# Optimization experiments

Hardware: AMD Instinct MI355X
Metric: run time of the kernel (lower is better)

## Reference

```python
import jax, jax.numpy as jnp
import numpy as np

# Simulation constants (from module source)
RADIUS = 0.1
DT = 1.0 / 60.0
MAX_VEL = 0.5 * 0.1 / DT
NUM_ITERATIONS = 3
RELAXATION = 1.0
VISCOSITY = 60.0
DENSITY_REST = 17510.1
STIFFNESS = 2.99e-11
EPS = 1e-8
_SPIKY_C = 15.0 / (np.pi * RADIUS ** 6)  # spiky kernel normalization


def _cap_magnitude(A, cap):
    # torch: vv = cap/(||A||+1e-4); vv = min(vv, 1); A*vv
    vv = jnp.sqrt(jnp.sum(A * A, axis=-1, keepdims=True))
    s = jnp.minimum(cap / (vv + 1e-4), 1.0)
    return A * s


def setup_inputs() -> dict:
    key = jax.random.key(0)
    k1, k2 = jax.random.split(key)
    N = 4096
    locs = jax.random.uniform(k1, (1, N, 3), dtype=jnp.float32)  # unit box
    vel = 0.1 * jax.random.normal(k2, (1, N, 3), dtype=jnp.float32)
    return {"locs": locs, "vel": vel}


def _pairwise(pred):
    # pred: [B,N,3] -> diff [B,N,N,3], stable distance d [B,N,N], neighbor mask
    diff = pred[:, :, None, :] - pred[:, None, :, :]
    d2 = jnp.sum(diff * diff, axis=-1)
    d = jnp.sqrt(d2 + EPS)
    mask = (d < RADIUS) & (d2 > 1e-12)  # exclude self (include_self=False)
    return diff, d, mask


def reference(locs, vel):
    gravity = jnp.array([0.0, -9.8, 0.0], dtype=locs.dtype)
    # external forces + velocity clamp
    vel = vel + gravity * DT
    vel = _cap_magnitude(vel, MAX_VEL)
    pred = locs + DT * vel

    # position-based density constraint solver iterations
    for _ in range(NUM_ITERATIONS):
        diff, d, mask = _pairwise(pred)
        w = jnp.where(mask, _SPIKY_C * (RADIUS - d) ** 3, 0.0)       # spiky
        rho = jnp.sum(w, axis=-1)                                     # [B,N]
        lam = -(rho - DENSITY_REST) * STIFFNESS                       # [B,N]
        dw = jnp.where(mask, -3.0 * _SPIKY_C * (RADIUS - d) ** 2, 0.0)  # dspiky
        coef = (lam[:, :, None] + lam[:, None, :]) * dw / d           # [B,N,N]
        delta = jnp.einsum('bij,bijd->bid', coef, diff)
        pred = pred + delta / RELAXATION

    new_vel = (pred - locs) / DT

    # XSPH viscosity smoothing: dv_i = sum_j w_ij (v_j - v_i)
    _, d, mask = _pairwise(pred)
    w = jnp.where(mask, _SPIKY_C * (RADIUS - d) ** 3, 0.0)
    wsum = jnp.sum(w, axis=-1, keepdims=True)
    dv = jnp.einsum('bij,bjd->bid', w, new_vel) - wsum * new_vel
    new_vel = new_vel + VISCOSITY * DT * dv / DENSITY_REST
    new_vel = _cap_magnitude(new_vel, MAX_VEL)
    return pred, new_vel
```

## Files before the change

kernel.cpp:

```cpp
#include <hip/hip_runtime.h>
#include <math.h>

#define NMAX 4096
#define N4   (NMAX/4)


constexpr float RADIUS       = 0.1f;
constexpr float DT           = 1.0f / 60.0f;
constexpr float MAX_VEL      = 3.0f;
constexpr float VISCOSITY    = 60.0f;
constexpr float DENSITY_REST = 17510.1f;
constexpr float STIFFNESS    = 2.99e-11f;
constexpr float EPS          = 1e-8f;
constexpr float SPIKY_C      = (float)(15.0 / (3.14159265358979323846 * 1e-6));

__device__ __forceinline__ float elem(const float4& v, int c) {
    return reinterpret_cast<const float*>(&v)[c];
}

__global__ void k_predict(const float* __restrict__ locs, const float* __restrict__ vel,
                          float* __restrict__ px, float* __restrict__ py, float* __restrict__ pz,
                          int n) {
    int i = blockIdx.x * blockDim.x + threadIdx.x;
    if (i >= n) return;
    float vx = vel[3*i+0];
    float vy = vel[3*i+1] - 9.8f * DT;
    float vz = vel[3*i+2];
    float vv = sqrtf(vx*vx + vy*vy + vz*vz);
    float s  = fminf(MAX_VEL / (vv + 1e-4f), 1.0f);
    vx *= s; vy *= s; vz *= s;
    px[i] = locs[3*i+0] + DT * vx;
    py[i] = locs[3*i+1] + DT * vy;
    pz[i] = locs[3*i+2] + DT * vz;
}

__global__ __launch_bounds__(256) void k_rho(const float4* __restrict__ px, const float4* __restrict__ py,
                                             const float4* __restrict__ pz, float* __restrict__ Lam, int n) {
    __shared__ float4 sx[N4], sy[N4], sz[N4];
    int n4 = n >> 2;
    for (int idx = threadIdx.x; idx < n4; idx += 256) {
        sx[idx] = px[idx]; sy[idx] = py[idx]; sz[idx] = pz[idx];
    }
    __syncthreads();
    const int wave = threadIdx.x >> 6, lane = threadIdx.x & 63;
    const int i0 = blockIdx.x * 8 + wave * 2;
    if (i0 >= n) return;
    const float* fx = (const float*)sx; const float* fy = (const float*)sy; const float* fz = (const float*)sz;
    const float xi0 = fx[i0],   yi0 = fy[i0],   zi0 = fz[i0];
    const float xi1 = fx[i0+1], yi1 = fy[i0+1], zi1 = fz[i0+1];
    float S0 = 0.f, S1 = 0.f;
    for (int k = lane; k < n4; k += 64) {
        float4 X = sx[k], Y = sy[k], Z = sz[k];
#pragma unroll
        for (int c = 0; c < 4; ++c) {
            float xj = elem(X,c), yj = elem(Y,c), zj = elem(Z,c);
            {
                float dx = xi0-xj, dy = yi0-yj, dz = zi0-zj;
                float d2 = fmaf(dx,dx,EPS); d2 = fmaf(dy,dy,d2); d2 = fmaf(dz,dz,d2);
                float t  = fmaxf(RADIUS - __builtin_amdgcn_sqrtf(d2), 0.f);
                S0 = fmaf(t*t, t, S0);
            }
            {
                float dx = xi1-xj, dy = yi1-yj, dz = zi1-zj;
                float d2 = fmaf(dx,dx,EPS); d2 = fmaf(dy,dy,d2); d2 = fmaf(dz,dz,d2);
                float t  = fmaxf(RADIUS - __builtin_amdgcn_sqrtf(d2), 0.f);
                S1 = fmaf(t*t, t, S1);
            }
        }
    }
    for (int off = 32; off > 0; off >>= 1) {
        S0 += __shfl_down(S0, off);
        S1 += __shfl_down(S1, off);
    }
    if (lane == 0) {
        const float ts  = RADIUS - __builtin_amdgcn_sqrtf(EPS);
        const float TS3 = ts*ts*ts;
        const float k3  = 3.f * SPIKY_C * STIFFNESS;
        Lam[i0]   = k3 * (SPIKY_C * (S0 - TS3) - DENSITY_REST);
        Lam[i0+1] = k3 * (SPIKY_C * (S1 - TS3) - DENSITY_REST);
    }
}

__global__ __launch_bounds__(256) void k_delta(const float4* __restrict__ px, const float4* __restrict__ py,
                                               const float4* __restrict__ pz, const float4* __restrict__ Lm,
                                               float* __restrict__ qx, float* __restrict__ qy, float* __restrict__ qz,
                                               const float* __restrict__ locs,
                                               float* __restrict__ out_pred,
                                               float* __restrict__ vnx, float* __restrict__ vny, float* __restrict__ vnz,
                                               int n) {
    __shared__ float4 sx[N4], sy[N4], sz[N4], sl[N4];
    int n4 = n >> 2;
    for (int idx = threadIdx.x; idx < n4; idx += 256) {
        sx[idx] = px[idx]; sy[idx] = py[idx]; sz[idx] = pz[idx]; sl[idx] = Lm[idx];
    }
    __syncthreads();
    const int wave = threadIdx.x >> 6, lane = threadIdx.x & 63;
    const int i0 = blockIdx.x * 8 + wave * 2;
    if (i0 >= n) return;
    const float* fx = (const float*)sx; const float* fy = (const float*)sy;
    const float* fz = (const float*)sz; const float* fl = (const float*)sl;
    const float xi0 = fx[i0],   yi0 = fy[i0],   zi0 = fz[i0],   L0 = fl[i0];
    const float xi1 = fx[i0+1], yi1 = fy[i0+1], zi1 = fz[i0+1], L1 = fl[i0+1];
    float ax0=0.f, ay0=0.f, az0=0.f, ax1=0.f, ay1=0.f, az1=0.f;
    for (int k = lane; k < n4; k += 64) {
        float4 X = sx[k], Y = sy[k], Z = sz[k], L = sl[k];
#pragma unroll
        for (int c = 0; c < 4; ++c) {
            float xj = elem(X,c), yj = elem(Y,c), zj = elem(Z,c), Lj = elem(L,c);
            {
                float dx = xi0-xj, dy = yi0-yj, dz = zi0-zj;
                float d2 = fmaf(dx,dx,EPS); d2 = fmaf(dy,dy,d2); d2 = fmaf(dz,dz,d2);
                float rinv = __builtin_amdgcn_rsqf(d2);
                float t  = fmaxf(RADIUS - d2*rinv, 0.f);
                float cf = (L0 + Lj) * (t*t) * rinv;
                ax0 = fmaf(cf, dx, ax0); ay0 = fmaf(cf, dy, ay0); az0 = fmaf(cf, dz, az0);
            }
            {
                float dx = xi1-xj, dy = yi1-yj, dz = zi1-zj;
                float d2 = fmaf(dx,dx,EPS); d2 = fmaf(dy,dy,d2); d2 = fmaf(dz,dz,d2);
                float rinv = __builtin_amdgcn_rsqf(d2);
                float t  = fmaxf(RADIUS - d2*rinv, 0.f);
                float cf = (L1 + Lj) * (t*t) * rinv;
                ax1 = fmaf(cf, dx, ax1); ay1 = fmaf(cf, dy, ay1); az1 = fmaf(cf, dz, az1);
            }
        }
    }
    for (int off = 32; off > 0; off >>= 1) {
        ax0 += __shfl_down(ax0, off); ay0 += __shfl_down(ay0, off); az0 += __shfl_down(az0, off);
        ax1 += __shfl_down(ax1, off); ay1 += __shfl_down(ay1, off); az1 += __shfl_down(az1, off);
    }
    if (lane == 0) {
#pragma unroll
        for (int u = 0; u < 2; ++u) {
            int i = i0 + u;
            float nx_ = (u ? xi1+ax1 : xi0+ax0);
            float ny_ = (u ? yi1+ay1 : yi0+ay0);
            float nz_ = (u ? zi1+az1 : zi0+az0);
            qx[i] = nx_; qy[i] = ny_; qz[i] = nz_;
            if (out_pred) {
                out_pred[3*i+0] = nx_; out_pred[3*i+1] = ny_; out_pred[3*i+2] = nz_;
                vnx[i] = (nx_ - locs[3*i+0]) * (1.0f/DT);
                vny[i] = (ny_ - locs[3*i+1]) * (1.0f/DT);
                vnz[i] = (nz_ - locs[3*i+2]) * (1.0f/DT);
            }
        }
    }
}

__global__ __launch_bounds__(256) void k_visc(const float4* __restrict__ px, const float4* __restrict__ py,
                                              const float4* __restrict__ pz,
                                              const float4* __restrict__ vx, const float4* __restrict__ vy,
                                              const float4* __restrict__ vz,
                                              float* __restrict__ out, int n) {
    __shared__ float4 sx[N4/2], sy[N4/2], sz[N4/2], svx[N4/2], svy[N4/2], svz[N4/2];
    const int wave = threadIdx.x >> 6, lane = threadIdx.x & 63;
    const int i0 = blockIdx.x * 8 + wave * 2;
    const float* fpx = (const float*)px; const float* fpy = (const float*)py; const float* fpz = (const float*)pz;
    const float* fvx = (const float*)vx; const float* fvy = (const float*)vy; const float* fvz = (const float*)vz;
    const float xi0 = fpx[i0],   yi0 = fpy[i0],   zi0 = fpz[i0];
    const float xi1 = fpx[i0+1], yi1 = fpy[i0+1], zi1 = fpz[i0+1];
    const float vix0 = fvx[i0],   viy0 = fvy[i0],   viz0 = fvz[i0];
    const float vix1 = fvx[i0+1], viy1 = fvy[i0+1], viz1 = fvz[i0+1];
    float ws0=0.f, ax0=0.f, ay0=0.f, az0=0.f;
    float ws1=0.f, ax1=0.f, ay1=0.f, az1=0.f;
    const int n8 = n >> 3;
    for (int ch = 0; ch < 2; ++ch) {
        __syncthreads();
        for (int idx = threadIdx.x; idx < n8; idx += 256) {
            sx[idx]  = px[ch*n8+idx]; sy[idx]  = py[ch*n8+idx]; sz[idx]  = pz[ch*n8+idx];
            svx[idx] = vx[ch*n8+idx]; svy[idx] = vy[ch*n8+idx]; svz[idx] = vz[ch*n8+idx];
        }
        __syncthreads();
        for (int k = lane; k < n8; k += 64) {
            float4 X = sx[k], Y = sy[k], Z = sz[k], VX = svx[k], VY = svy[k], VZ = svz[k];
#pragma unroll
            for (int c = 0; c < 4; ++c) {
                float xj = elem(X,c), yj = elem(Y,c), zj = elem(Z,c);
                float vxj = elem(VX,c), vyj = elem(VY,c), vzj = elem(VZ,c);
                {
                    float dx = xi0-xj, dy = yi0-yj, dz = zi0-zj;
                    float d2 = fmaf(dx,dx,EPS); d2 = fmaf(dy,dy,d2); d2 = fmaf(dz,dz,d2);
                    float t  = fmaxf(RADIUS - __builtin_amdgcn_sqrtf(d2), 0.f);
                    float w  = t*t*t;
                    ws0 += w;
                    ax0 = fmaf(w, vxj, ax0); ay0 = fmaf(w, vyj, ay0); az0 = fmaf(w, vzj, az0);
                }
                {
                    float dx = xi1-xj, dy = yi1-yj, dz = zi1-zj;
                    float d2 = fmaf(dx,dx,EPS); d2 = fmaf(dy,dy,d2); d2 = fmaf(dz,dz,d2);
                    float t  = fmaxf(RADIUS - __builtin_amdgcn_sqrtf(d2), 0.f);
                    float w  = t*t*t;
                    ws1 += w;
                    ax1 = fmaf(w, vxj, ax1); ay1 = fmaf(w, vyj, ay1); az1 = fmaf(w, vzj, az1);
                }
            }
        }
    }
    for (int off = 32; off > 0; off >>= 1) {
        ws0 += __shfl_down(ws0, off); ax0 += __shfl_down(ax0, off);
        ay0 += __shfl_down(ay0, off); az0 += __shfl_down(az0, off);
        ws1 += __shfl_down(ws1, off); ax1 += __shfl_down(ax1, off);
        ay1 += __shfl_down(ay1, off); az1 += __shfl_down(az1, off);
    }
    if (lane == 0 && i0 < n) {
        constexpr float K = VISCOSITY * DT / DENSITY_REST;
        const float KC = K * SPIKY_C;
#pragma unroll
        for (int u = 0; u < 2; ++u) {
            int i = i0 + u;
            float vix = (u ? vix1 : vix0), viy = (u ? viy1 : viy0), viz = (u ? viz1 : viz0);
            float sw  = (u ? ws1 : ws0);
            float sax = (u ? ax1 : ax0), say = (u ? ay1 : ay0), saz = (u ? az1 : az0);
            float nvx = vix + KC * (sax - sw * vix);
            float nvy = viy + KC * (say - sw * viy);
            float nvz = viz + KC * (saz - sw * viz);
            float vv = sqrtf(nvx*nvx + nvy*nvy + nvz*nvz);
            float s  = fminf(MAX_VEL / (vv + 1e-4f), 1.0f);
            out[3*n + 3*i + 0] = nvx * s;
            out[3*n + 3*i + 1] = nvy * s;
            out[3*n + 3*i + 2] = nvz * s;
        }
    }
}

extern "C" void kernel_launch(void* const* d_in, const int* in_sizes, int n_in,
                              void* d_out, int out_size, void* d_ws, size_t ws_size,
                              hipStream_t stream) {
    const float* locs = (const float*)d_in[0];
    const float* vel  = (const float*)d_in[1];
    float* out = (float*)d_out;
    int n = in_sizes[0] / 3;

    float* w = (float*)d_ws;
    float* p0x = w;          float* p0y = p0x + n;  float* p0z = p0y + n;
    float* p1x = p0z + n;    float* p1y = p1x + n;  float* p1z = p1y + n;
    float* lam = p1z + n;
    float* vnx = lam + n;    float* vny = vnx + n;  float* vnz = vny + n;

    int nb = n / 8;

    k_predict<<<(n + 255) / 256, 256, 0, stream>>>(locs, vel, p0x, p0y, p0z, n);

    k_rho<<<nb, 256, 0, stream>>>((const float4*)p0x, (const float4*)p0y, (const float4*)p0z, lam, n);
    k_delta<<<nb, 256, 0, stream>>>((const float4*)p0x, (const float4*)p0y, (const float4*)p0z,
                                    (const float4*)lam, p1x, p1y, p1z,
                                    locs, nullptr, nullptr, nullptr, nullptr, n);
    k_rho<<<nb, 256, 0, stream>>>((const float4*)p1x, (const float4*)p1y, (const float4*)p1z, lam, n);
    k_delta<<<nb, 256, 0, stream>>>((const float4*)p1x, (const float4*)p1y, (const float4*)p1z,
                                    (const float4*)lam, p0x, p0y, p0z,
                                    locs, nullptr, nullptr, nullptr, nullptr, n);
    k_rho<<<nb, 256, 0, stream>>>((const float4*)p0x, (const float4*)p0y, (const float4*)p0z, lam, n);
    k_delta<<<nb, 256, 0, stream>>>((const float4*)p0x, (const float4*)p0y, (const float4*)p0z,
                                    (const float4*)lam, p1x, p1y, p1z,
                                    locs, out, vnx, vny, vnz, n);
    k_visc<<<nb, 256, 0, stream>>>((const float4*)p1x, (const float4*)p1y, (const float4*)p1z,
                                   (const float4*)vnx, (const float4*)vny, (const float4*)vnz, out, n);
}
```

Measured before the change: 123.9 us.

## Fuse predict, solver iterations and viscosity into one cooperative kernel

Merges the predict, the three density/delta iterations and the XSPH viscosity kernels into a single cooperative kernel that uses grid-wide syncs between phases. It also updates positions in place, replacing the double buffer. The aim is to remove eight kernel launches and the gaps between them. In exchange it adds seven grid barriers and a fixed 64KB shared-memory footprint per block, which may lower occupancy. It also relies on all n/8 blocks being co-resident for the cooperative launch.

```diff
diff --git a/kernel.cpp b/kernel.cpp
--- a/kernel.cpp
+++ b/kernel.cpp
@@ -1,5 +1,8 @@
 #include <hip/hip_runtime.h>
+#include <hip/hip_cooperative_groups.h>
 #include <math.h>
+
+namespace cg = cooperative_groups;
 
 #define NMAX 4096
 #define N4   (NMAX/4)
@@ -18,167 +21,163 @@
     return reinterpret_cast<const float*>(&v)[c];
 }
 
-__global__ void k_predict(const float* __restrict__ locs, const float* __restrict__ vel,
-                          float* __restrict__ px, float* __restrict__ py, float* __restrict__ pz,
-                          int n) {
-    int i = blockIdx.x * blockDim.x + threadIdx.x;
-    if (i >= n) return;
-    float vx = vel[3*i+0];
-    float vy = vel[3*i+1] - 9.8f * DT;
-    float vz = vel[3*i+2];
-    float vv = sqrtf(vx*vx + vy*vy + vz*vz);
-    float s  = fminf(MAX_VEL / (vv + 1e-4f), 1.0f);
-    vx *= s; vy *= s; vz *= s;
-    px[i] = locs[3*i+0] + DT * vx;
-    py[i] = locs[3*i+1] + DT * vy;
-    pz[i] = locs[3*i+2] + DT * vz;
-}
-
-__global__ __launch_bounds__(256) void k_rho(const float4* __restrict__ px, const float4* __restrict__ py,
-                                             const float4* __restrict__ pz, float* __restrict__ Lam, int n) {
-    __shared__ float4 sx[N4], sy[N4], sz[N4];
-    int n4 = n >> 2;
-    for (int idx = threadIdx.x; idx < n4; idx += 256) {
-        sx[idx] = px[idx]; sy[idx] = py[idx]; sz[idx] = pz[idx];
-    }
-    __syncthreads();
-    const int wave = threadIdx.x >> 6, lane = threadIdx.x & 63;
-    const int i0 = blockIdx.x * 8 + wave * 2;
-    if (i0 >= n) return;
-    const float* fx = (const float*)sx; const float* fy = (const float*)sy; const float* fz = (const float*)sz;
-    const float xi0 = fx[i0],   yi0 = fy[i0],   zi0 = fz[i0];
-    const float xi1 = fx[i0+1], yi1 = fy[i0+1], zi1 = fz[i0+1];
-    float S0 = 0.f, S1 = 0.f;
-    for (int k = lane; k < n4; k += 64) {
-        float4 X = sx[k], Y = sy[k], Z = sz[k];
-#pragma unroll
-        for (int c = 0; c < 4; ++c) {
-            float xj = elem(X,c), yj = elem(Y,c), zj = elem(Z,c);
-            {
-                float dx = xi0-xj, dy = yi0-yj, dz = zi0-zj;
-                float d2 = fmaf(dx,dx,EPS); d2 = fmaf(dy,dy,d2); d2 = fmaf(dz,dz,d2);
-                float t  = fmaxf(RADIUS - __builtin_amdgcn_sqrtf(d2), 0.f);
-                S0 = fmaf(t*t, t, S0);
-            }
-            {
-                float dx = xi1-xj, dy = yi1-yj, dz = zi1-zj;
-                float d2 = fmaf(dx,dx,EPS); d2 = fmaf(dy,dy,d2); d2 = fmaf(dz,dz,d2);
-                float t  = fmaxf(RADIUS - __builtin_amdgcn_sqrtf(d2), 0.f);
-                S1 = fmaf(t*t, t, S1);
-            }
-        }
-    }
-    for (int off = 32; off > 0; off >>= 1) {
-        S0 += __shfl_down(S0, off);
-        S1 += __shfl_down(S1, off);
-    }
-    if (lane == 0) {
-        const float ts  = RADIUS - __builtin_amdgcn_sqrtf(EPS);
-        const float TS3 = ts*ts*ts;
-        const float k3  = 3.f * SPIKY_C * STIFFNESS;
-        Lam[i0]   = k3 * (SPIKY_C * (S0 - TS3) - DENSITY_REST);
-        Lam[i0+1] = k3 * (SPIKY_C * (S1 - TS3) - DENSITY_REST);
-    }
-}
-
-__global__ __launch_bounds__(256) void k_delta(const float4* __restrict__ px, const float4* __restrict__ py,
-                                               const float4* __restrict__ pz, const float4* __restrict__ Lm,
-                                               float* __restrict__ qx, float* __restrict__ qy, float* __restrict__ qz,
-                                               const float* __restrict__ locs,
-                                               float* __restrict__ out_pred,
-                                               float* __restrict__ vnx, float* __restrict__ vny, float* __restrict__ vnz,
-                                               int n) {
-    __shared__ float4 sx[N4], sy[N4], sz[N4], sl[N4];
-    int n4 = n >> 2;
-    for (int idx = threadIdx.x; idx < n4; idx += 256) {
-        sx[idx] = px[idx]; sy[idx] = py[idx]; sz[idx] = pz[idx]; sl[idx] = Lm[idx];
-    }
-    __syncthreads();
-    const int wave = threadIdx.x >> 6, lane = threadIdx.x & 63;
-    const int i0 = blockIdx.x * 8 + wave * 2;
-    if (i0 >= n) return;
-    const float* fx = (const float*)sx; const float* fy = (const float*)sy;
-    const float* fz = (const float*)sz; const float* fl = (const float*)sl;
-    const float xi0 = fx[i0],   yi0 = fy[i0],   zi0 = fz[i0],   L0 = fl[i0];
-    const float xi1 = fx[i0+1], yi1 = fy[i0+1], zi1 = fz[i0+1], L1 = fl[i0+1];
-    float ax0=0.f, ay0=0.f, az0=0.f, ax1=0.f, ay1=0.f, az1=0.f;
-    for (int k = lane; k < n4; k += 64) {
-        float4 X = sx[k], Y = sy[k], Z = sz[k], L = sl[k];
-#pragma unroll
-        for (int c = 0; c < 4; ++c) {
-            float xj = elem(X,c), yj = elem(Y,c), zj = elem(Z,c), Lj = elem(L,c);
-            {
-                float dx = xi0-xj, dy = yi0-yj, dz = zi0-zj;
-                float d2 = fmaf(dx,dx,EPS); d2 = fmaf(dy,dy,d2); d2 = fmaf(dz,dz,d2);
-                float rinv = __builtin_amdgcn_rsqf(d2);
-                float t  = fmaxf(RADIUS - d2*rinv, 0.f);
-                float cf = (L0 + Lj) * (t*t) * rinv;
-                ax0 = fmaf(cf, dx, ax0); ay0 = fmaf(cf, dy, ay0); az0 = fmaf(cf, dz, az0);
-            }
-            {
-                float dx = xi1-xj, dy = yi1-yj, dz = zi1-zj;
-                float d2 = fmaf(dx,dx,EPS); d2 = fmaf(dy,dy,d2); d2 = fmaf(dz,dz,d2);
-                float rinv = __builtin_amdgcn_rsqf(d2);
-                float t  = fmaxf(RADIUS - d2*rinv, 0.f);
-                float cf = (L1 + Lj) * (t*t) * rinv;
-                ax1 = fmaf(cf, dx, ax1); ay1 = fmaf(cf, dy, ay1); az1 = fmaf(cf, dz, az1);
-            }
-        }
-    }
-    for (int off = 32; off > 0; off >>= 1) {
-        ax0 += __shfl_down(ax0, off); ay0 += __shfl_down(ay0, off); az0 += __shfl_down(az0, off);
-        ax1 += __shfl_down(ax1, off); ay1 += __shfl_down(ay1, off); az1 += __shfl_down(az1, off);
-    }
-    if (lane == 0) {
-#pragma unroll
-        for (int u = 0; u < 2; ++u) {
-            int i = i0 + u;
-            float nx_ = (u ? xi1+ax1 : xi0+ax0);
-            float ny_ = (u ? yi1+ay1 : yi0+ay0);
-            float nz_ = (u ? zi1+az1 : zi0+az0);
-            qx[i] = nx_; qy[i] = ny_; qz[i] = nz_;
-            if (out_pred) {
-                out_pred[3*i+0] = nx_; out_pred[3*i+1] = ny_; out_pred[3*i+2] = nz_;
-                vnx[i] = (nx_ - locs[3*i+0]) * (1.0f/DT);
-                vny[i] = (ny_ - locs[3*i+1]) * (1.0f/DT);
-                vnz[i] = (nz_ - locs[3*i+2]) * (1.0f/DT);
-            }
-        }
-    }
-}
-
-__global__ __launch_bounds__(256) void k_visc(const float4* __restrict__ px, const float4* __restrict__ py,
-                                              const float4* __restrict__ pz,
-                                              const float4* __restrict__ vx, const float4* __restrict__ vy,
-                                              const float4* __restrict__ vz,
-                                              float* __restrict__ out, int n) {
-    __shared__ float4 sx[N4/2], sy[N4/2], sz[N4/2], svx[N4/2], svy[N4/2], svz[N4/2];
-    const int wave = threadIdx.x >> 6, lane = threadIdx.x & 63;
-    const int i0 = blockIdx.x * 8 + wave * 2;
-    const float* fpx = (const float*)px; const float* fpy = (const float*)py; const float* fpz = (const float*)pz;
-    const float* fvx = (const float*)vx; const float* fvy = (const float*)vy; const float* fvz = (const float*)vz;
-    const float xi0 = fpx[i0],   yi0 = fpy[i0],   zi0 = fpz[i0];
-    const float xi1 = fpx[i0+1], yi1 = fpy[i0+1], zi1 = fpz[i0+1];
-    const float vix0 = fvx[i0],   viy0 = fvy[i0],   viz0 = fvz[i0];
-    const float vix1 = fvx[i0+1], viy1 = fvy[i0+1], viz1 = fvz[i0+1];
+__global__ __launch_bounds__(256) void k_fused(
+        const float* __restrict__ locs, const float* __restrict__ vel,
+        float* __restrict__ px, float* __restrict__ py, float* __restrict__ pz,
+        float* __restrict__ lam,
+        float* __restrict__ vnx, float* __restrict__ vny, float* __restrict__ vnz,
+        float* __restrict__ out, int n) {
+    cg::grid_group grid = cg::this_grid();
+    __shared__ float4 smem[4 * N4];
+    float4* sx = smem;
+    float4* sy = smem + N4;
+    float4* sz = smem + 2 * N4;
+    float4* sl = smem + 3 * N4;
+    const int tid  = threadIdx.x;
+    const int wave = tid >> 6, lane = tid & 63;
+    const int i0   = blockIdx.x * 8 + wave * 2;
+    const int n4   = n >> 2;
+
+    {
+        int i = blockIdx.x * 256 + tid;
+        if (i < n) {
+            float vx = vel[3*i+0];
+            float vy = vel[3*i+1] - 9.8f * DT;
+            float vz = vel[3*i+2];
+            float vv = sqrtf(vx*vx + vy*vy + vz*vz);
+            float s  = fminf(MAX_VEL / (vv + 1e-4f), 1.0f);
+            px[i] = locs[3*i+0] + DT * vx * s;
+            py[i] = locs[3*i+1] + DT * vy * s;
+            pz[i] = locs[3*i+2] + DT * vz * s;
+        }
+    }
+    grid.sync();
+
+    for (int it = 0; it < 3; ++it) {
+        for (int idx = tid; idx < n4; idx += 256) {
+            sx[idx] = ((const float4*)px)[idx];
+            sy[idx] = ((const float4*)py)[idx];
+            sz[idx] = ((const float4*)pz)[idx];
+        }
+        __syncthreads();
+
+        const float* fx = (const float*)sx; const float* fy = (const float*)sy;
+        const float* fz = (const float*)sz; const float* fl = (const float*)sl;
+        const float xi0 = fx[i0],   yi0 = fy[i0],   zi0 = fz[i0];
+        const float xi1 = fx[i0+1], yi1 = fy[i0+1], zi1 = fz[i0+1];
+
+        float S0 = 0.f, S1 = 0.f;
+        for (int k = lane; k < n4; k += 64) {
+            float4 X = sx[k], Y = sy[k], Z = sz[k];
+#pragma unroll
+            for (int c = 0; c < 4; ++c) {
+                float xj = elem(X,c), yj = elem(Y,c), zj = elem(Z,c);
+                {
+                    float dx = xi0-xj, dy = yi0-yj, dz = zi0-zj;
+                    float d2 = fmaf(dx,dx,EPS); d2 = fmaf(dy,dy,d2); d2 = fmaf(dz,dz,d2);
+                    float t  = fmaxf(RADIUS - __builtin_amdgcn_sqrtf(d2), 0.f);
+                    S0 = fmaf(t*t, t, S0);
+                }
+                {
+                    float dx = xi1-xj, dy = yi1-yj, dz = zi1-zj;
+                    float d2 = fmaf(dx,dx,EPS); d2 = fmaf(dy,dy,d2); d2 = fmaf(dz,dz,d2);
+                    float t  = fmaxf(RADIUS - __builtin_amdgcn_sqrtf(d2), 0.f);
+                    S1 = fmaf(t*t, t, S1);
+                }
+            }
+        }
+        for (int off = 32; off > 0; off >>= 1) {
+            S0 += __shfl_down(S0, off);
+            S1 += __shfl_down(S1, off);
+        }
+        if (lane == 0) {
+            const float ts  = RADIUS - __builtin_amdgcn_sqrtf(EPS);
+            const float TS3 = ts*ts*ts;
+            const float k3  = 3.f * SPIKY_C * STIFFNESS;
+            lam[i0]   = k3 * (SPIKY_C * (S0 - TS3) - DENSITY_REST);
+            lam[i0+1] = k3 * (SPIKY_C * (S1 - TS3) - DENSITY_REST);
+        }
+        grid.sync();
+
+        for (int idx = tid; idx < n4; idx += 256) sl[idx] = ((const float4*)lam)[idx];
+        __syncthreads();
+
+        const float L0 = fl[i0], L1 = fl[i0+1];
+        float ax0=0.f, ay0=0.f, az0=0.f, ax1=0.f, ay1=0.f, az1=0.f;
+        for (int k = lane; k < n4; k += 64) {
+            float4 X = sx[k], Y = sy[k], Z = sz[k], L = sl[k];
+#pragma unroll
+            for (int c = 0; c < 4; ++c) {
+                float xj = elem(X,c), yj = elem(Y,c), zj = elem(Z,c), Lj = elem(L,c);
+                {
+                    float dx = xi0-xj, dy = yi0-yj, dz = zi0-zj;
+                    float d2 = fmaf(dx,dx,EPS); d2 = fmaf(dy,dy,d2); d2 = fmaf(dz,dz,d2);
+                    float rinv = __builtin_amdgcn_rsqf(d2);
+                    float t  = fmaxf(RADIUS - d2*rinv, 0.f);
+                    float cf = (L0 + Lj) * (t*t) * rinv;
+                    ax0 = fmaf(cf, dx, ax0); ay0 = fmaf(cf, dy, ay0); az0 = fmaf(cf, dz, az0);
+                }
+                {
+                    float dx = xi1-xj, dy = yi1-yj, dz = zi1-zj;
+                    float d2 = fmaf(dx,dx,EPS); d2 = fmaf(dy,dy,d2); d2 = fmaf(dz,dz,d2);
+                    float rinv = __builtin_amdgcn_rsqf(d2);
+                    float t  = fmaxf(RADIUS - d2*rinv, 0.f);
+                    float cf = (L1 + Lj) * (t*t) * rinv;
+                    ax1 = fmaf(cf, dx, ax1); ay1 = fmaf(cf, dy, ay1); az1 = fmaf(cf, dz, az1);
+                }
+            }
+        }
+        for (int off = 32; off > 0; off >>= 1) {
+            ax0 += __shfl_down(ax0, off); ay0 += __shfl_down(ay0, off); az0 += __shfl_down(az0, off);
+            ax1 += __shfl_down(ax1, off); ay1 += __shfl_down(ay1, off); az1 += __shfl_down(az1, off);
+        }
+        if (lane == 0) {
+#pragma unroll
+            for (int u = 0; u < 2; ++u) {
+                int i = i0 + u;
+                float nx_ = (u ? xi1+ax1 : xi0+ax0);
+                float ny_ = (u ? yi1+ay1 : yi0+ay0);
+                float nz_ = (u ? zi1+az1 : zi0+az0);
+                px[i] = nx_; py[i] = ny_; pz[i] = nz_;
+                if (it == 2) {
+                    out[3*i+0] = nx_; out[3*i+1] = ny_; out[3*i+2] = nz_;
+                    vnx[i] = (nx_ - locs[3*i+0]) * (1.0f/DT);
+                    vny[i] = (ny_ - locs[3*i+1]) * (1.0f/DT);
+                    vnz[i] = (nz_ - locs[3*i+2]) * (1.0f/DT);
+                }
+            }
+        }
+        grid.sync();
+    }
+
+    const int n8 = n >> 3;
+    float4* cx  = smem;            float4* cy  = smem + n8;     float4* cz  = smem + 2*n8;
+    float4* cvx = smem + 3*n8;     float4* cvy = smem + 4*n8;   float4* cvz = smem + 5*n8;
+    const float Xi0 = px[i0],   Yi0 = py[i0],   Zi0 = pz[i0];
+    const float Xi1 = px[i0+1], Yi1 = py[i0+1], Zi1 = pz[i0+1];
+    const float vix0 = vnx[i0],   viy0 = vny[i0],   viz0 = vnz[i0];
+    const float vix1 = vnx[i0+1], viy1 = vny[i0+1], viz1 = vnz[i0+1];
     float ws0=0.f, ax0=0.f, ay0=0.f, az0=0.f;
     float ws1=0.f, ax1=0.f, ay1=0.f, az1=0.f;
-    const int n8 = n >> 3;
     for (int ch = 0; ch < 2; ++ch) {
         __syncthreads();
-        for (int idx = threadIdx.x; idx < n8; idx += 256) {
-            sx[idx]  = px[ch*n8+idx]; sy[idx]  = py[ch*n8+idx]; sz[idx]  = pz[ch*n8+idx];
-            svx[idx] = vx[ch*n8+idx]; svy[idx] = vy[ch*n8+idx]; svz[idx] = vz[ch*n8+idx];
+        for (int idx = tid; idx < n8; idx += 256) {
+            cx[idx]  = ((const float4*)px)[ch*n8+idx];
+            cy[idx]  = ((const float4*)py)[ch*n8+idx];
+            cz[idx]  = ((const float4*)pz)[ch*n8+idx];
+            cvx[idx] = ((const float4*)vnx)[ch*n8+idx];
+            cvy[idx] = ((const float4*)vny)[ch*n8+idx];
+            cvz[idx] = ((const float4*)vnz)[ch*n8+idx];
         }
         __syncthreads();
         for (int k = lane; k < n8; k += 64) {
-            float4 X = sx[k], Y = sy[k], Z = sz[k], VX = svx[k], VY = svy[k], VZ = svz[k];
+            float4 X = cx[k], Y = cy[k], Z = cz[k], VX = cvx[k], VY = cvy[k], VZ = cvz[k];
 #pragma unroll
             for (int c = 0; c < 4; ++c) {
                 float xj = elem(X,c), yj = elem(Y,c), zj = elem(Z,c);
                 float vxj = elem(VX,c), vyj = elem(VY,c), vzj = elem(VZ,c);
                 {
-                    float dx = xi0-xj, dy = yi0-yj, dz = zi0-zj;
+                    float dx = Xi0-xj, dy = Yi0-yj, dz = Zi0-zj;
                     float d2 = fmaf(dx,dx,EPS); d2 = fmaf(dy,dy,d2); d2 = fmaf(dz,dz,d2);
                     float t  = fmaxf(RADIUS - __builtin_amdgcn_sqrtf(d2), 0.f);
                     float w  = t*t*t;
@@ -186,7 +185,7 @@
                     ax0 = fmaf(w, vxj, ax0); ay0 = fmaf(w, vyj, ay0); az0 = fmaf(w, vzj, az0);
                 }
                 {
-                    float dx = xi1-xj, dy = yi1-yj, dz = zi1-zj;
+                    float dx = Xi1-xj, dy = Yi1-yj, dz = Zi1-zj;
                     float d2 = fmaf(dx,dx,EPS); d2 = fmaf(dy,dy,d2); d2 = fmaf(dz,dz,d2);
                     float t  = fmaxf(RADIUS - __builtin_amdgcn_sqrtf(d2), 0.f);
                     float w  = t*t*t;
@@ -202,7 +201,7 @@
         ws1 += __shfl_down(ws1, off); ax1 += __shfl_down(ax1, off);
         ay1 += __shfl_down(ay1, off); az1 += __shfl_down(az1, off);
     }
-    if (lane == 0 && i0 < n) {
+    if (lane == 0) {
         constexpr float K = VISCOSITY * DT / DENSITY_REST;
         const float KC = K * SPIKY_C;
 #pragma unroll
@@ -232,27 +231,12 @@
     int n = in_sizes[0] / 3;
 
     float* w = (float*)d_ws;
-    float* p0x = w;          float* p0y = p0x + n;  float* p0z = p0y + n;
-    float* p1x = p0z + n;    float* p1y = p1x + n;  float* p1z = p1y + n;
-    float* lam = p1z + n;
-    float* vnx = lam + n;    float* vny = vnx + n;  float* vnz = vny + n;
-
-    int nb = n / 8;
-
-    k_predict<<<(n + 255) / 256, 256, 0, stream>>>(locs, vel, p0x, p0y, p0z, n);
-
-    k_rho<<<nb, 256, 0, stream>>>((const float4*)p0x, (const float4*)p0y, (const float4*)p0z, lam, n);
-    k_delta<<<nb, 256, 0, stream>>>((const float4*)p0x, (const float4*)p0y, (const float4*)p0z,
-                                    (const float4*)lam, p1x, p1y, p1z,
-                                    locs, nullptr, nullptr, nullptr, nullptr, n);
-    k_rho<<<nb, 256, 0, stream>>>((const float4*)p1x, (const float4*)p1y, (const float4*)p1z, lam, n);
-    k_delta<<<nb, 256, 0, stream>>>((const float4*)p1x, (const float4*)p1y, (const float4*)p1z,
-                                    (const float4*)lam, p0x, p0y, p0z,
-                                    locs, nullptr, nullptr, nullptr, nullptr, n);
-    k_rho<<<nb, 256, 0, stream>>>((const float4*)p0x, (const float4*)p0y, (const float4*)p0z, lam, n);
-    k_delta<<<nb, 256, 0, stream>>>((const float4*)p0x, (const float4*)p0y, (const float4*)p0z,
-                                    (const float4*)lam, p1x, p1y, p1z,
-                                    locs, out, vnx, vny, vnz, n);
-    k_visc<<<nb, 256, 0, stream>>>((const float4*)p1x, (const float4*)p1y, (const float4*)p1z,
-                                   (const float4*)vnx, (const float4*)vny, (const float4*)vnz, out, n);
+    float* px  = w;        float* py  = px + n;   float* pz  = py + n;
+    float* lam = pz + n;
+    float* vnx = lam + n;  float* vny = vnx + n;  float* vnz = vny + n;
+
+    void* args[] = { (void*)&locs, (void*)&vel, (void*)&px, (void*)&py, (void*)&pz,
+                     (void*)&lam, (void*)&vnx, (void*)&vny, (void*)&vnz,
+                     (void*)&out, (void*)&n };
+    hipLaunchCooperativeKernel((const void*)k_fused, dim3(n / 8), dim3(256), args, 0, stream);
 }
```

Result: slower. 437.5 us (+253.2%).

## Fuse predict step into first solver kernels and use one particle per wave

Applied to the files above, without the earlier changes.

Removes the separate predict kernel: the first rho and delta kernels each recompute predicted positions from locs and vel directly into shared memory. Blocks grow to 512 threads with eight waves and one particle per wave instead of two, keeping the grid at n/8 blocks, so there are twice as many waves per block. This saves one launch and a global round trip. In exchange the prediction work is redone in every block, and each wave now reuses each shared-memory load of a neighbour for only one particle instead of two.

```diff
diff --git a/kernel.cpp b/kernel.cpp
--- a/kernel.cpp
+++ b/kernel.cpp
@@ -18,208 +18,195 @@
     return reinterpret_cast<const float*>(&v)[c];
 }
 
-__global__ void k_predict(const float* __restrict__ locs, const float* __restrict__ vel,
-                          float* __restrict__ px, float* __restrict__ py, float* __restrict__ pz,
-                          int n) {
-    int i = blockIdx.x * blockDim.x + threadIdx.x;
-    if (i >= n) return;
-    float vx = vel[3*i+0];
-    float vy = vel[3*i+1] - 9.8f * DT;
-    float vz = vel[3*i+2];
-    float vv = sqrtf(vx*vx + vy*vy + vz*vz);
-    float s  = fminf(MAX_VEL / (vv + 1e-4f), 1.0f);
-    vx *= s; vy *= s; vz *= s;
-    px[i] = locs[3*i+0] + DT * vx;
-    py[i] = locs[3*i+1] + DT * vy;
-    pz[i] = locs[3*i+2] + DT * vz;
-}
-
-__global__ __launch_bounds__(256) void k_rho(const float4* __restrict__ px, const float4* __restrict__ py,
-                                             const float4* __restrict__ pz, float* __restrict__ Lam, int n) {
-    __shared__ float4 sx[N4], sy[N4], sz[N4];
-    int n4 = n >> 2;
-    for (int idx = threadIdx.x; idx < n4; idx += 256) {
-        sx[idx] = px[idx]; sy[idx] = py[idx]; sz[idx] = pz[idx];
-    }
-    __syncthreads();
-    const int wave = threadIdx.x >> 6, lane = threadIdx.x & 63;
-    const int i0 = blockIdx.x * 8 + wave * 2;
-    if (i0 >= n) return;
+__device__ __forceinline__ void predict_to_lds(const float4* __restrict__ locs4,
+                                               const float4* __restrict__ vel4,
+                                               float4* sx, float4* sy, float4* sz,
+                                               int n4, int tid, int nthreads) {
+    for (int g = tid; g < n4; g += nthreads) {
+        float lo[12], ve[12];
+        *(float4*)&lo[0] = locs4[3*g];   *(float4*)&lo[4] = locs4[3*g+1]; *(float4*)&lo[8] = locs4[3*g+2];
+        *(float4*)&ve[0] = vel4[3*g];    *(float4*)&ve[4] = vel4[3*g+1];  *(float4*)&ve[8] = vel4[3*g+2];
+        float X[4], Y[4], Z[4];
+#pragma unroll
+        for (int p = 0; p < 4; ++p) {
+            float vx = ve[3*p], vy = ve[3*p+1] - 9.8f * DT, vz = ve[3*p+2];
+            float vv = sqrtf(vx*vx + vy*vy + vz*vz);
+            float s  = fminf(MAX_VEL / (vv + 1e-4f), 1.0f);
+            X[p] = lo[3*p]   + DT * vx * s;
+            Y[p] = lo[3*p+1] + DT * vy * s;
+            Z[p] = lo[3*p+2] + DT * vz * s;
+        }
+        sx[g] = make_float4(X[0], X[1], X[2], X[3]);
+        sy[g] = make_float4(Y[0], Y[1], Y[2], Y[3]);
+        sz[g] = make_float4(Z[0], Z[1], Z[2], Z[3]);
+    }
+}
+
+__device__ __forceinline__ void rho_body(const float4* sx, const float4* sy, const float4* sz,
+                                         float* __restrict__ lam, int n4, int i, int lane) {
     const float* fx = (const float*)sx; const float* fy = (const float*)sy; const float* fz = (const float*)sz;
-    const float xi0 = fx[i0],   yi0 = fy[i0],   zi0 = fz[i0];
-    const float xi1 = fx[i0+1], yi1 = fy[i0+1], zi1 = fz[i0+1];
-    float S0 = 0.f, S1 = 0.f;
+    const float xi = fx[i], yi = fy[i], zi = fz[i];
+    float S = 0.f;
     for (int k = lane; k < n4; k += 64) {
         float4 X = sx[k], Y = sy[k], Z = sz[k];
 #pragma unroll
         for (int c = 0; c < 4; ++c) {
-            float xj = elem(X,c), yj = elem(Y,c), zj = elem(Z,c);
-            {
-                float dx = xi0-xj, dy = yi0-yj, dz = zi0-zj;
-                float d2 = fmaf(dx,dx,EPS); d2 = fmaf(dy,dy,d2); d2 = fmaf(dz,dz,d2);
-                float t  = fmaxf(RADIUS - __builtin_amdgcn_sqrtf(d2), 0.f);
-                S0 = fmaf(t*t, t, S0);
-            }
-            {
-                float dx = xi1-xj, dy = yi1-yj, dz = zi1-zj;
-                float d2 = fmaf(dx,dx,EPS); d2 = fmaf(dy,dy,d2); d2 = fmaf(dz,dz,d2);
-                float t  = fmaxf(RADIUS - __builtin_amdgcn_sqrtf(d2), 0.f);
-                S1 = fmaf(t*t, t, S1);
-            }
-        }
-    }
-    for (int off = 32; off > 0; off >>= 1) {
-        S0 += __shfl_down(S0, off);
-        S1 += __shfl_down(S1, off);
-    }
+            float dx = xi - elem(X,c), dy = yi - elem(Y,c), dz = zi - elem(Z,c);
+            float d2 = fmaf(dx,dx,EPS); d2 = fmaf(dy,dy,d2); d2 = fmaf(dz,dz,d2);
+            float t  = fmaxf(RADIUS - __builtin_amdgcn_sqrtf(d2), 0.f);
+            S = fmaf(t*t, t, S);
+        }
+    }
+    for (int off = 32; off > 0; off >>= 1) S += __shfl_down(S, off);
     if (lane == 0) {
         const float ts  = RADIUS - __builtin_amdgcn_sqrtf(EPS);
         const float TS3 = ts*ts*ts;
         const float k3  = 3.f * SPIKY_C * STIFFNESS;
-        Lam[i0]   = k3 * (SPIKY_C * (S0 - TS3) - DENSITY_REST);
-        Lam[i0+1] = k3 * (SPIKY_C * (S1 - TS3) - DENSITY_REST);
-    }
-}
-
-__global__ __launch_bounds__(256) void k_delta(const float4* __restrict__ px, const float4* __restrict__ py,
-                                               const float4* __restrict__ pz, const float4* __restrict__ Lm,
-                                               float* __restrict__ qx, float* __restrict__ qy, float* __restrict__ qz,
-                                               const float* __restrict__ locs,
-                                               float* __restrict__ out_pred,
-                                               float* __restrict__ vnx, float* __restrict__ vny, float* __restrict__ vnz,
-                                               int n) {
-    __shared__ float4 sx[N4], sy[N4], sz[N4], sl[N4];
-    int n4 = n >> 2;
-    for (int idx = threadIdx.x; idx < n4; idx += 256) {
-        sx[idx] = px[idx]; sy[idx] = py[idx]; sz[idx] = pz[idx]; sl[idx] = Lm[idx];
-    }
-    __syncthreads();
-    const int wave = threadIdx.x >> 6, lane = threadIdx.x & 63;
-    const int i0 = blockIdx.x * 8 + wave * 2;
-    if (i0 >= n) return;
+        lam[i] = k3 * (SPIKY_C * (S - TS3) - DENSITY_REST);
+    }
+}
+
+__device__ __forceinline__ void delta_body(const float4* sx, const float4* sy, const float4* sz,
+                                           const float4* sl,
+                                           float* __restrict__ qx, float* __restrict__ qy, float* __restrict__ qz,
+                                           const float* __restrict__ locs,
+                                           float* __restrict__ out_pred,
+                                           float* __restrict__ vnx, float* __restrict__ vny, float* __restrict__ vnz,
+                                           int n4, int i, int lane) {
     const float* fx = (const float*)sx; const float* fy = (const float*)sy;
     const float* fz = (const float*)sz; const float* fl = (const float*)sl;
-    const float xi0 = fx[i0],   yi0 = fy[i0],   zi0 = fz[i0],   L0 = fl[i0];
-    const float xi1 = fx[i0+1], yi1 = fy[i0+1], zi1 = fz[i0+1], L1 = fl[i0+1];
-    float ax0=0.f, ay0=0.f, az0=0.f, ax1=0.f, ay1=0.f, az1=0.f;
+    const float xi = fx[i], yi = fy[i], zi = fz[i], Li = fl[i];
+    float ax = 0.f, ay = 0.f, az = 0.f;
     for (int k = lane; k < n4; k += 64) {
         float4 X = sx[k], Y = sy[k], Z = sz[k], L = sl[k];
 #pragma unroll
         for (int c = 0; c < 4; ++c) {
-            float xj = elem(X,c), yj = elem(Y,c), zj = elem(Z,c), Lj = elem(L,c);
-            {
-                float dx = xi0-xj, dy = yi0-yj, dz = zi0-zj;
-                float d2 = fmaf(dx,dx,EPS); d2 = fmaf(dy,dy,d2); d2 = fmaf(dz,dz,d2);
-                float rinv = __builtin_amdgcn_rsqf(d2);
-                float t  = fmaxf(RADIUS - d2*rinv, 0.f);
-                float cf = (L0 + Lj) * (t*t) * rinv;
-                ax0 = fmaf(cf, dx, ax0); ay0 = fmaf(cf, dy, ay0); az0 = fmaf(cf, dz, az0);
-            }
-            {
-                float dx = xi1-xj, dy = yi1-yj, dz = zi1-zj;
-                float d2 = fmaf(dx,dx,EPS); d2 = fmaf(dy,dy,d2); d2 = fmaf(dz,dz,d2);
-                float rinv = __builtin_amdgcn_rsqf(d2);
-                float t  = fmaxf(RADIUS - d2*rinv, 0.f);
-                float cf = (L1 + Lj) * (t*t) * rinv;
-                ax1 = fmaf(cf, dx, ax1); ay1 = fmaf(cf, dy, ay1); az1 = fmaf(cf, dz, az1);
-            }
+            float dx = xi - elem(X,c), dy = yi - elem(Y,c), dz = zi - elem(Z,c);
+            float d2 = fmaf(dx,dx,EPS); d2 = fmaf(dy,dy,d2); d2 = fmaf(dz,dz,d2);
+            float rinv = __builtin_amdgcn_rsqf(d2);
+            float t  = fmaxf(RADIUS - d2*rinv, 0.f);
+            float cf = (Li + elem(L,c)) * (t*t) * rinv;
+            ax = fmaf(cf, dx, ax); ay = fmaf(cf, dy, ay); az = fmaf(cf, dz, az);
         }
     }
     for (int off = 32; off > 0; off >>= 1) {
-        ax0 += __shfl_down(ax0, off); ay0 += __shfl_down(ay0, off); az0 += __shfl_down(az0, off);
-        ax1 += __shfl_down(ax1, off); ay1 += __shfl_down(ay1, off); az1 += __shfl_down(az1, off);
+        ax += __shfl_down(ax, off); ay += __shfl_down(ay, off); az += __shfl_down(az, off);
     }
     if (lane == 0) {
-#pragma unroll
-        for (int u = 0; u < 2; ++u) {
-            int i = i0 + u;
-            float nx_ = (u ? xi1+ax1 : xi0+ax0);
-            float ny_ = (u ? yi1+ay1 : yi0+ay0);
-            float nz_ = (u ? zi1+az1 : zi0+az0);
-            qx[i] = nx_; qy[i] = ny_; qz[i] = nz_;
-            if (out_pred) {
-                out_pred[3*i+0] = nx_; out_pred[3*i+1] = ny_; out_pred[3*i+2] = nz_;
-                vnx[i] = (nx_ - locs[3*i+0]) * (1.0f/DT);
-                vny[i] = (ny_ - locs[3*i+1]) * (1.0f/DT);
-                vnz[i] = (nz_ - locs[3*i+2]) * (1.0f/DT);
-            }
-        }
-    }
-}
-
-__global__ __launch_bounds__(256) void k_visc(const float4* __restrict__ px, const float4* __restrict__ py,
-                                              const float4* __restrict__ pz,
-                                              const float4* __restrict__ vx, const float4* __restrict__ vy,
-                                              const float4* __restrict__ vz,
-                                              float* __restrict__ out, int n) {
-    __shared__ float4 sx[N4/2], sy[N4/2], sz[N4/2], svx[N4/2], svy[N4/2], svz[N4/2];
+        float nx_ = xi + ax, ny_ = yi + ay, nz_ = zi + az;
+        qx[i] = nx_; qy[i] = ny_; qz[i] = nz_;
+        if (out_pred) {
+            out_pred[3*i+0] = nx_; out_pred[3*i+1] = ny_; out_pred[3*i+2] = nz_;
+            vnx[i] = (nx_ - locs[3*i+0]) * (1.0f/DT);
+            vny[i] = (ny_ - locs[3*i+1]) * (1.0f/DT);
+            vnz[i] = (nz_ - locs[3*i+2]) * (1.0f/DT);
+        }
+    }
+}
+
+
+__global__ __launch_bounds__(512, 4) void k_rho_first(const float4* __restrict__ locs4,
+                                                      const float4* __restrict__ vel4,
+                                                      float* __restrict__ lam, int n) {
+    __shared__ float4 sx[N4], sy[N4], sz[N4];
+    const int n4 = n >> 2;
+    predict_to_lds(locs4, vel4, sx, sy, sz, n4, threadIdx.x, 512);
+    __syncthreads();
+    rho_body(sx, sy, sz, lam, n4, blockIdx.x * 8 + (threadIdx.x >> 6), threadIdx.x & 63);
+}
+
+__global__ __launch_bounds__(512, 4) void k_delta_first(const float4* __restrict__ locs4,
+                                                        const float4* __restrict__ vel4,
+                                                        const float4* __restrict__ Lm,
+                                                        float* __restrict__ qx, float* __restrict__ qy,
+                                                        float* __restrict__ qz, int n) {
+    __shared__ float4 sx[N4], sy[N4], sz[N4], sl[N4];
+    const int n4 = n >> 2;
+    predict_to_lds(locs4, vel4, sx, sy, sz, n4, threadIdx.x, 512);
+    for (int idx = threadIdx.x; idx < n4; idx += 512) sl[idx] = Lm[idx];
+    __syncthreads();
+    delta_body(sx, sy, sz, sl, qx, qy, qz, nullptr, nullptr, nullptr, nullptr, nullptr,
+               n4, blockIdx.x * 8 + (threadIdx.x >> 6), threadIdx.x & 63);
+}
+
+__global__ __launch_bounds__(512, 4) void k_rho(const float4* __restrict__ px, const float4* __restrict__ py,
+                                                const float4* __restrict__ pz, float* __restrict__ lam, int n) {
+    __shared__ float4 sx[N4], sy[N4], sz[N4];
+    const int n4 = n >> 2;
+    for (int idx = threadIdx.x; idx < n4; idx += 512) {
+        sx[idx] = px[idx]; sy[idx] = py[idx]; sz[idx] = pz[idx];
+    }
+    __syncthreads();
+    rho_body(sx, sy, sz, lam, n4, blockIdx.x * 8 + (threadIdx.x >> 6), threadIdx.x & 63);
+}
+
+__global__ __launch_bounds__(512, 4) void k_delta(const float4* __restrict__ px, const float4* __restrict__ py,
+                                                  const float4* __restrict__ pz, const float4* __restrict__ Lm,
+                                                  float* __restrict__ qx, float* __restrict__ qy, float* __restrict__ qz,
+                                                  const float* __restrict__ locs,
+                                                  float* __restrict__ out_pred,
+                                                  float* __restrict__ vnx, float* __restrict__ vny, float* __restrict__ vnz,
+                                                  int n) {
+    __shared__ float4 sx[N4], sy[N4], sz[N4], sl[N4];
+    const int n4 = n >> 2;
+    for (int idx = threadIdx.x; idx < n4; idx += 512) {
+        sx[idx] = px[idx]; sy[idx] = py[idx]; sz[idx] = pz[idx]; sl[idx] = Lm[idx];
+    }
+    __syncthreads();
+    delta_body(sx, sy, sz, sl, qx, qy, qz, locs, out_pred, vnx, vny, vnz,
+               n4, blockIdx.x * 8 + (threadIdx.x >> 6), threadIdx.x & 63);
+}
+
+__global__ __launch_bounds__(512, 4) void k_visc(const float4* __restrict__ px, const float4* __restrict__ py,
+                                                 const float4* __restrict__ pz,
+                                                 const float4* __restrict__ vx, const float4* __restrict__ vy,
+                                                 const float4* __restrict__ vz,
+                                                 float* __restrict__ out, int n) {
+    __shared__ float4 cs[6][N4/2];
     const int wave = threadIdx.x >> 6, lane = threadIdx.x & 63;
-    const int i0 = blockIdx.x * 8 + wave * 2;
+    const int i = blockIdx.x * 8 + wave;
     const float* fpx = (const float*)px; const float* fpy = (const float*)py; const float* fpz = (const float*)pz;
     const float* fvx = (const float*)vx; const float* fvy = (const float*)vy; const float* fvz = (const float*)vz;
-    const float xi0 = fpx[i0],   yi0 = fpy[i0],   zi0 = fpz[i0];
-    const float xi1 = fpx[i0+1], yi1 = fpy[i0+1], zi1 = fpz[i0+1];
-    const float vix0 = fvx[i0],   viy0 = fvy[i0],   viz0 = fvz[i0];
-    const float vix1 = fvx[i0+1], viy1 = fvy[i0+1], viz1 = fvz[i0+1];
-    float ws0=0.f, ax0=0.f, ay0=0.f, az0=0.f;
-    float ws1=0.f, ax1=0.f, ay1=0.f, az1=0.f;
+    const float xi = fpx[i], yi = fpy[i], zi = fpz[i];
+    const float vix = fvx[i], viy = fvy[i], viz = fvz[i];
+    float ws = 0.f, ax = 0.f, ay = 0.f, az = 0.f;
     const int n8 = n >> 3;
     for (int ch = 0; ch < 2; ++ch) {
         __syncthreads();
-        for (int idx = threadIdx.x; idx < n8; idx += 256) {
-            sx[idx]  = px[ch*n8+idx]; sy[idx]  = py[ch*n8+idx]; sz[idx]  = pz[ch*n8+idx];
-            svx[idx] = vx[ch*n8+idx]; svy[idx] = vy[ch*n8+idx]; svz[idx] = vz[ch*n8+idx];
+        for (int idx = threadIdx.x; idx < n8; idx += 512) {
+            cs[0][idx] = px[ch*n8+idx]; cs[1][idx] = py[ch*n8+idx]; cs[2][idx] = pz[ch*n8+idx];
+            cs[3][idx] = vx[ch*n8+idx]; cs[4][idx] = vy[ch*n8+idx]; cs[5][idx] = vz[ch*n8+idx];
         }
         __syncthreads();
         for (int k = lane; k < n8; k += 64) {
-            float4 X = sx[k], Y = sy[k], Z = sz[k], VX = svx[k], VY = svy[k], VZ = svz[k];
+            float4 X = cs[0][k], Y = cs[1][k], Z = cs[2][k];
+            float4 VX = cs[3][k], VY = cs[4][k], VZ = cs[5][k];
 #pragma unroll
             for (int c = 0; c < 4; ++c) {
-                float xj = elem(X,c), yj = elem(Y,c), zj = elem(Z,c);
-                float vxj = elem(VX,c), vyj = elem(VY,c), vzj = elem(VZ,c);
-                {
-                    float dx = xi0-xj, dy = yi0-yj, dz = zi0-zj;
-                    float d2 = fmaf(dx,dx,EPS); d2 = fmaf(dy,dy,d2); d2 = fmaf(dz,dz,d2);
-                    float t  = fmaxf(RADIUS - __builtin_amdgcn_sqrtf(d2), 0.f);
-                    float w  = t*t*t;
-                    ws0 += w;
-                    ax0 = fmaf(w, vxj, ax0); ay0 = fmaf(w, vyj, ay0); az0 = fmaf(w, vzj, az0);
-                }
-                {
-                    float dx = xi1-xj, dy = yi1-yj, dz = zi1-zj;
-                    float d2 = fmaf(dx,dx,EPS); d2 = fmaf(dy,dy,d2); d2 = fmaf(dz,dz,d2);
-                    float t  = fmaxf(RADIUS - __builtin_amdgcn_sqrtf(d2), 0.f);
-                    float w  = t*t*t;
-                    ws1 += w;
-                    ax1 = fmaf(w, vxj, ax1); ay1 = fmaf(w, vyj, ay1); az1 = fmaf(w, vzj, az1);
-                }
+                float dx = xi - elem(X,c), dy = yi - elem(Y,c), dz = zi - elem(Z,c);
+                float d2 = fmaf(dx,dx,EPS); d2 = fmaf(dy,dy,d2); d2 = fmaf(dz,dz,d2);
+                float t  = fmaxf(RADIUS - __builtin_amdgcn_sqrtf(d2), 0.f);
+                float w  = t*t*t;
+                ws += w;
+                ax = fmaf(w, elem(VX,c), ax); ay = fmaf(w, elem(VY,c), ay); az = fmaf(w, elem(VZ,c), az);
             }
         }
     }
     for (int off = 32; off > 0; off >>= 1) {
-        ws0 += __shfl_down(ws0, off); ax0 += __shfl_down(ax0, off);
-        ay0 += __shfl_down(ay0, off); az0 += __shfl_down(az0, off);
-        ws1 += __shfl_down(ws1, off); ax1 += __shfl_down(ax1, off);
-        ay1 += __shfl_down(ay1, off); az1 += __shfl_down(az1, off);
-    }
-    if (lane == 0 && i0 < n) {
+        ws += __shfl_down(ws, off); ax += __shfl_down(ax, off);
+        ay += __shfl_down(ay, off); az += __shfl_down(az, off);
+    }
+    if (lane == 0) {
         constexpr float K = VISCOSITY * DT / DENSITY_REST;
         const float KC = K * SPIKY_C;
-#pragma unroll
-        for (int u = 0; u < 2; ++u) {
-            int i = i0 + u;
-            float vix = (u ? vix1 : vix0), viy = (u ? viy1 : viy0), viz = (u ? viz1 : viz0);
-            float sw  = (u ? ws1 : ws0);
-            float sax = (u ? ax1 : ax0), say = (u ? ay1 : ay0), saz = (u ? az1 : az0);
-            float nvx = vix + KC * (sax - sw * vix);
-            float nvy = viy + KC * (say - sw * viy);
-            float nvz = viz + KC * (saz - sw * viz);
-            float vv = sqrtf(nvx*nvx + nvy*nvy + nvz*nvz);
-            float s  = fminf(MAX_VEL / (vv + 1e-4f), 1.0f);
-            out[3*n + 3*i + 0] = nvx * s;
-            out[3*n + 3*i + 1] = nvy * s;
-            out[3*n + 3*i + 2] = nvz * s;
-        }
+        float nvx = vix + KC * (ax - ws * vix);
+        float nvy = viy + KC * (ay - ws * viy);
+        float nvz = viz + KC * (az - ws * viz);
+        float vv = sqrtf(nvx*nvx + nvy*nvy + nvz*nvz);
+        float s  = fminf(MAX_VEL / (vv + 1e-4f), 1.0f);
+        out[3*n + 3*i + 0] = nvx * s;
+        out[3*n + 3*i + 1] = nvy * s;
+        out[3*n + 3*i + 2] = nvz * s;
     }
 }
 
@@ -228,31 +215,29 @@
                               hipStream_t stream) {
     const float* locs = (const float*)d_in[0];
     const float* vel  = (const float*)d_in[1];
+    const float4* locs4 = (const float4*)locs;
+    const float4* vel4  = (const float4*)vel;
     float* out = (float*)d_out;
     int n = in_sizes[0] / 3;
 
     float* w = (float*)d_ws;
-    float* p0x = w;          float* p0y = p0x + n;  float* p0z = p0y + n;
-    float* p1x = p0z + n;    float* p1y = p1x + n;  float* p1z = p1y + n;
-    float* lam = p1z + n;
-    float* vnx = lam + n;    float* vny = vnx + n;  float* vnz = vny + n;
+    float* pAx = w;        float* pAy = pAx + n;  float* pAz = pAy + n;
+    float* pBx = pAz + n;  float* pBy = pBx + n;  float* pBz = pBy + n;
+    float* lam = pBz + n;
+    float* vnx = lam + n;  float* vny = vnx + n;  float* vnz = vny + n;
 
     int nb = n / 8;
 
-    k_predict<<<(n + 255) / 256, 256, 0, stream>>>(locs, vel, p0x, p0y, p0z, n);
-
-    k_rho<<<nb, 256, 0, stream>>>((const float4*)p0x, (const float4*)p0y, (const float4*)p0z, lam, n);
-    k_delta<<<nb, 256, 0, stream>>>((const float4*)p0x, (const float4*)p0y, (const float4*)p0z,
-                                    (const float4*)lam, p1x, p1y, p1z,
-                                    locs, nullptr, nullptr, nullptr, nullptr, n);
-    k_rho<<<nb, 256, 0, stream>>>((const float4*)p1x, (const float4*)p1y, (const float4*)p1z, lam, n);
-    k_delta<<<nb, 256, 0, stream>>>((const float4*)p1x, (const float4*)p1y, (const float4*)p1z,
-                                    (const float4*)lam, p0x, p0y, p0z,
-                                    locs, nullptr, nullptr, nullptr, nullptr, n);
-    k_rho<<<nb, 256, 0, stream>>>((const float4*)p0x, (const float4*)p0y, (const float4*)p0z, lam, n);
-    k_delta<<<nb, 256, 0, stream>>>((const float4*)p0x, (const float4*)p0y, (const float4*)p0z,
-                                    (const float4*)lam, p1x, p1y, p1z,
+    k_rho_first<<<nb, 512, 0, stream>>>(locs4, vel4, lam, n);
+    k_delta_first<<<nb, 512, 0, stream>>>(locs4, vel4, (const float4*)lam, pAx, pAy, pAz, n);
+    k_rho<<<nb, 512, 0, stream>>>((const float4*)pAx, (const float4*)pAy, (const float4*)pAz, lam, n);
+    k_delta<<<nb, 512, 0, stream>>>((const float4*)pAx, (const float4*)pAy, (const float4*)pAz,
+                                    (const float4*)lam, pBx, pBy, pBz,
+                                    nullptr, nullptr, nullptr, nullptr, nullptr, n);
+    k_rho<<<nb, 512, 0, stream>>>((const float4*)pBx, (const float4*)pBy, (const float4*)pBz, lam, n);
+    k_delta<<<nb, 512, 0, stream>>>((const float4*)pBx, (const float4*)pBy, (const float4*)pBz,
+                                    (const float4*)lam, pAx, pAy, pAz,
                                     locs, out, vnx, vny, vnz, n);
-    k_visc<<<nb, 256, 0, stream>>>((const float4*)p1x, (const float4*)p1y, (const float4*)p1z,
+    k_visc<<<nb, 512, 0, stream>>>((const float4*)pAx, (const float4*)pAy, (const float4*)pAz,
                                    (const float4*)vnx, (const float4*)vny, (const float4*)vnz, out, n);
 }
```

Result: no change. 125.8 us (+1.6%).
